# Kernel tuning notes

Measured on AMD Instinct MI355X. Metric: run time of the kernel, lower is better.

## Reference

```python
import jax, jax.numpy as jnp
import numpy as np

THRESH = 0.5   # global `thresh` used by ActFun
LENS = 0.5     # global `lens` (surrogate width)
DECAY = 0.25   # LIFNode init_decay
INV_STD = 1.0 / float(np.sqrt(1.0 + 1e-5))  # BN eval: running_mean=0, running_var=1
HEADS = 8
WINDOW = 8

@jax.custom_vjp
def act_fun(x):
    return (x > THRESH).astype(x.dtype)

def _act_fwd(x):
    return act_fun(x), x

def _act_bwd(x, g):
    temp = (jnp.abs(x - THRESH) < LENS).astype(g.dtype) / (2.0 * LENS)
    return (g * temp,)

act_fun.defvjp(_act_fwd, _act_bwd)

def lif(x):
    # x: [T, ...]; mem = x[0]; mem_t = mem_{t-1}*decay*(1-spike_{t-1}.detach()) + x_t
    spike0 = act_fun(x[0])
    def step(carry, xi):
        mem_prev, spike_prev = carry
        mem = mem_prev * DECAY * (1.0 - jax.lax.stop_gradient(spike_prev)) + xi
        spike = act_fun(mem)
        return (mem, spike), spike
    _, spikes = jax.lax.scan(step, (x[0], spike0), x[1:])
    return jnp.concatenate([spike0[None], spikes], axis=0)

def bn_eval(x, gamma, beta):
    # BatchNorm2d eval over channel D (last dim of [T,B,L,D]) with default running stats
    return x * (INV_STD * gamma) + beta

def linear(x, w, b):
    # torch nn.Linear: y = x @ w.T + b, w: [out, in]
    return jnp.einsum('tbld,ed->tble', x, w) + b


def setup_inputs() -> dict:
    key = jax.random.key(0)
    ks = jax.random.split(key, 12)
    T, B, L, D = 4, 4, 1024, 512
    s = 0.02
    inp = {
        'x': jax.random.normal(ks[0], (T, B, L, D), dtype=jnp.float32),
        'pos_bias': jax.random.uniform(ks[1], (L, L), dtype=jnp.float32),
        'q_w': jax.random.normal(ks[2], (D, D), dtype=jnp.float32) * s,
        'q_b': jnp.zeros((D,), jnp.float32),
        'q_g': jnp.ones((D,), jnp.float32),
        'q_beta': jnp.zeros((D,), jnp.float32),
        'k_w': jax.random.normal(ks[3], (D, D), dtype=jnp.float32) * s,
        'k_b': jnp.zeros((D,), jnp.float32),
        'k_g': jnp.ones((D,), jnp.float32),
        'k_beta': jnp.zeros((D,), jnp.float32),
        'v_w': jax.random.normal(ks[4], (D, D), dtype=jnp.float32) * s,
        'v_b': jnp.zeros((D,), jnp.float32),
        'v_g': jnp.ones((D,), jnp.float32),
        'v_beta': jnp.zeros((D,), jnp.float32),
        'last_w': jax.random.normal(ks[5], (D, D), dtype=jnp.float32) * s,
        'last_b': jnp.zeros((D,), jnp.float32),
        'last_g': jnp.ones((D,), jnp.float32),
        'last_beta': jnp.zeros((D,), jnp.float32),
    }
    return inp


def reference(x, pos_bias, q_w, q_b, q_g, q_beta, k_w, k_b, k_g, k_beta,
              v_w, v_b, v_g, v_beta, last_w, last_b, last_g, last_beta):
    T, B, L, D = x.shape
    H = HEADS
    Dh = D // H
    # local causal band: keep pos_bias[i,j] only where 0 <= i-j < WINDOW
    i = jnp.arange(L)[:, None]
    j = jnp.arange(L)[None, :]
    band = ((i - j) >= 0) & ((i - j) < WINDOW)
    pb = jnp.where(band, pos_bias[:L, :L], 0.0)  # [L, L]

    xs = lif(x)  # first_lif
    q = lif(bn_eval(linear(xs, q_w, q_b), q_g, q_beta))
    k = lif(bn_eval(linear(xs, k_w, k_b), k_g, k_beta))
    v = lif(bn_eval(linear(xs, v_w, v_b), v_g, v_beta))

    # [T,B,L,D] -> [T,B,L,H,Dh] -> [B,H,L,T,Dh] -> [B,H,L,T*Dh]
    qh = q.reshape(T, B, L, H, Dh).transpose(1, 3, 2, 0, 4).reshape(B, H, L, T * Dh)
    kv = (k * v).reshape(T, B, L, H, Dh).transpose(1, 3, 2, 0, 4).reshape(B, H, L, T * Dh)

    attn = jnp.einsum('ij,bhjd->bhid', pb, kv)  # local-window positional mixing
    out = qh * attn
    out = out.reshape(B, H, L, T, Dh).transpose(3, 0, 2, 1, 4).reshape(T, B, L, D)
    out = lif(out)  # attn_lif
    out = bn_eval(linear(out, last_w, last_b), last_g, last_beta)
    return out
```

## Files before the change

### kernel.cpp

```cpp
#include <hip/hip_runtime.h>
#include <stdint.h>


#define T_ 4
#define B_ 4
#define L_ 1024
#define D_ 512
#define BI_ (B_*L_)
#define STRIDE4 (B_*L_*D_/4)
#define INV_STD 0.9999950000374997f
#define EPS_FLAG 1e-3f
#define LIST_CAP 5000000u

typedef unsigned int   u32;
typedef unsigned char  u8;
typedef int i32x4 __attribute__((ext_vector_type(4)));

static __device__ __forceinline__ float spike_of(float m) {
  return m > 0.5f ? 1.0f : 0.0f;
}

__device__ __forceinline__ void gll16(const void* g, void* l) {
  __builtin_amdgcn_global_load_lds(
      (const __attribute__((address_space(1))) u32*)g,
      (__attribute__((address_space(3))) u32*)l, 16, 0, 0);
}

__global__ __launch_bounds__(256) void k_wsplit(const float* __restrict__ qw,
    const float* __restrict__ kw, const float* __restrict__ vw,
    const float* __restrict__ lw, u8* __restrict__ Wq,
    float* __restrict__ scl, u32* __restrict__ cnt) {
  if (blockIdx.x == 0 && threadIdx.x == 0) *cnt = 0;
  int gid = blockIdx.x * 4 + (threadIdx.x >> 6);
  int mat = gid >> 9, e = gid & 511;
  int lane = threadIdx.x & 63;
  const float* W = mat == 0 ? qw : mat == 1 ? kw : mat == 2 ? vw : lw;
  const float4* w4 = (const float4*)(W + (size_t)e * 512 + lane * 8);
  float4 wa = w4[0], wb = w4[1];
  float w[8] = {wa.x, wa.y, wa.z, wa.w, wb.x, wb.y, wb.z, wb.w};
  float am = 0.f;
#pragma unroll
  for (int j = 0; j < 8; ++j) am = fmaxf(am, fabsf(w[j]));
#pragma unroll
  for (int off = 1; off < 64; off <<= 1)
    am = fmaxf(am, __shfl_xor(am, off, 64));
  float s1 = am > 0.f ? am * (1.0f / 127.0f) : 1.0f;
  float s2 = s1 * (1.0f / 254.0f);
  float inv1 = 1.0f / s1, inv2 = 1.0f / s2;
  u32 p1lo = 0, p1hi = 0, p2lo = 0, p2hi = 0;
#pragma unroll
  for (int j = 0; j < 8; ++j) {
    float q1 = rintf(w[j] * inv1);
    q1 = fminf(127.f, fmaxf(-127.f, q1));
    float r = w[j] - s1 * q1;
    float q2 = rintf(r * inv2);
    q2 = fminf(127.f, fmaxf(-127.f, q2));
    u32 b1 = (u32)(u8)(signed char)(int)q1;
    u32 b2 = (u32)(u8)(signed char)(int)q2;
    if (j < 4) { p1lo |= b1 << (j * 8); p2lo |= b2 << (j * 8); }
    else       { p1hi |= b1 << ((j - 4) * 8); p2hi |= b2 << ((j - 4) * 8); }
  }
  u8* base = Wq + (size_t)mat * 524288 + (size_t)e * 512 + lane * 8;
  *(uint2*)base             = make_uint2(p1lo, p1hi);
  *(uint2*)(base + 262144)  = make_uint2(p2lo, p2hi);
  if (lane == 0) {
    scl[mat * 1024 + e] = s1;
    scl[mat * 1024 + 512 + e] = s2;
  }
}

__global__ __launch_bounds__(256) void k_lif_first(const float* __restrict__ x,
                                                   u8* __restrict__ xsb) {
  int idx = blockIdx.x * 256 + threadIdx.x;
  if (idx >= STRIDE4) return;
  const int bi = idx >> 7, d4 = idx & 127;
  const float4* x4 = (const float4*)x;
  uchar4* o4 = (uchar4*)xsb;
  float m[4], s[4];
  float4 v = x4[idx];
  m[0] = v.x; m[1] = v.y; m[2] = v.z; m[3] = v.w;
#pragma unroll
  for (int c = 0; c < 4; ++c) s[c] = spike_of(m[c]);
  o4[(bi * 4 + 0) * 128 + d4] =
      make_uchar4((u8)s[0], (u8)s[1], (u8)s[2], (u8)s[3]);
#pragma unroll
  for (int t = 1; t < T_; ++t) {
    v = x4[idx + t * STRIDE4];
    float xv[4] = {v.x, v.y, v.z, v.w};
#pragma unroll
    for (int c = 0; c < 4; ++c) {
      m[c] = m[c] * 0.25f * (1.0f - s[c]) + xv[c];
      s[c] = spike_of(m[c]);
    }
    o4[(bi * 4 + t) * 128 + d4] =
        make_uchar4((u8)s[0], (u8)s[1], (u8)s[2], (u8)s[3]);
  }
}

__device__ __forceinline__ void gemm_core_i8(const u8* __restrict__ Ab,
    const u8* __restrict__ Wq2, int row0, int col0, int tid,
    unsigned char* sm, i32x4 (&acc0)[4][4], i32x4 (&acc1)[4][4]) {
  const u8* gsrc[12];
  int loff[12];
#pragma unroll
  for (int u = 0; u < 12; ++u) {
    if (u < 4) {
      int lin = u * 4096 + tid * 16;
      int r = lin >> 7, slot = (lin >> 4) & 7, gs = slot ^ (r & 7);
      gsrc[u] = Ab + (size_t)(row0 + r) * 512 + gs * 16;
      loff[u] = lin;
    } else {
      int lin = (u - 4) * 4096 + tid * 16;
      int plane = lin >> 14, l3 = lin & 16383;
      int r = l3 >> 7, slot = (l3 >> 4) & 7, gs = slot ^ (r & 7);
      gsrc[u] = Wq2 + (size_t)plane * 262144 + (size_t)(col0 + r) * 512 + gs * 16;
      loff[u] = 16384 + lin;
    }
  }
  const int lane = tid & 63;
  const int wid = tid >> 6;
  const int wr = wid >> 1, wc = wid & 1;
  const int la = lane & 15, lg = lane >> 4;

  int offA[4][2], offB[2][4][2];
#pragma unroll
  for (int mi = 0; mi < 4; ++mi) {
    int r = wr * 64 + mi * 16 + la;
#pragma unroll
    for (int ks = 0; ks < 2; ++ks)
      offA[mi][ks] = r * 128 + (((ks * 4 + lg) ^ (r & 7)) << 4);
  }
#pragma unroll
  for (int p = 0; p < 2; ++p)
#pragma unroll
    for (int ni = 0; ni < 4; ++ni) {
      int r = wc * 64 + ni * 16 + la;
#pragma unroll
      for (int ks = 0; ks < 2; ++ks)
        offB[p][ni][ks] = 16384 + p * 16384 + r * 128 +
                          (((ks * 4 + lg) ^ (r & 7)) << 4);
    }

#pragma unroll
  for (int a = 0; a < 4; ++a)
#pragma unroll
    for (int b = 0; b < 4; ++b) {
      acc0[a][b] = (i32x4){0, 0, 0, 0};
      acc1[a][b] = (i32x4){0, 0, 0, 0};
    }

  for (int k0 = 0; k0 < 4; ++k0) {
#pragma unroll
    for (int u = 0; u < 12; ++u) gll16(gsrc[u] + (k0 << 7), sm + loff[u]);
    __syncthreads();
    uint4 af[4][2];
#pragma unroll
    for (int mi = 0; mi < 4; ++mi)
#pragma unroll
      for (int ks = 0; ks < 2; ++ks)
        af[mi][ks] = *(const uint4*)(sm + offA[mi][ks]);
#pragma unroll
    for (int ks = 0; ks < 2; ++ks)
#pragma unroll
      for (int ni = 0; ni < 4; ++ni) {
        uint4 bf = *(const uint4*)(sm + offB[0][ni][ks]);
#pragma unroll
        for (int mi = 0; mi < 4; ++mi)
          acc0[mi][ni] = __builtin_amdgcn_mfma_i32_16x16x64_i8(
              __builtin_bit_cast(i32x4, af[mi][ks]),
              __builtin_bit_cast(i32x4, bf), acc0[mi][ni], 0, 0, 0);
      }
#pragma unroll
    for (int ks = 0; ks < 2; ++ks)
#pragma unroll
      for (int ni = 0; ni < 4; ++ni) {
        uint4 bf = *(const uint4*)(sm + offB[1][ni][ks]);
#pragma unroll
        for (int mi = 0; mi < 4; ++mi)
          acc1[mi][ni] = __builtin_amdgcn_mfma_i32_16x16x64_i8(
              __builtin_bit_cast(i32x4, af[mi][ks]),
              __builtin_bit_cast(i32x4, bf), acc1[mi][ni], 0, 0, 0);
      }
    __syncthreads();
  }
}

__global__ __launch_bounds__(256) void k_gemm_qkv(const u8* __restrict__ Ab,
    const u8* __restrict__ Wq, const float* __restrict__ scl,
    const float* __restrict__ qb2, const float* __restrict__ qg,
    const float* __restrict__ qbe,
    const float* __restrict__ kb2, const float* __restrict__ kg,
    const float* __restrict__ kbe,
    const float* __restrict__ vb2, const float* __restrict__ vg,
    const float* __restrict__ vbe,
    u8* __restrict__ qs, u8* __restrict__ ks, u8* __restrict__ vs,
    u32* __restrict__ list, u32* __restrict__ cnt) {
  __shared__ __align__(16) unsigned char sm[49152];
  const int tid = threadIdx.x;
  const int tz = blockIdx.z;
  const u8* Wp = Wq + (size_t)tz * 524288;
  const float* Bb = tz == 0 ? qb2 : tz == 1 ? kb2 : vb2;
  const float* Gg = tz == 0 ? qg  : tz == 1 ? kg  : vg;
  const float* Be = tz == 0 ? qbe : tz == 1 ? kbe : vbe;
  u8* S           = tz == 0 ? qs  : tz == 1 ? ks  : vs;

  int f = blockIdx.y * 4 + blockIdx.x;
  int tI = (f & 7) * 64 + (f >> 3);
  const int row0 = (tI >> 2) * 128;
  const int col0 = (tI & 3) * 128;

  i32x4 acc0[4][4], acc1[4][4];
  gemm_core_i8(Ab, Wp, row0, col0, tid, sm, acc0, acc1);

  const int lane = tid & 63;
  const int wid = tid >> 6;
  const int wr = wid >> 1, wc = wid & 1;
  const int la = lane & 15, lg = lane >> 4;

  u8* sm8 = sm;
#pragma unroll
  for (int ni = 0; ni < 4; ++ni) {
    int cl = wc * 64 + ni * 16 + la;
    int e = col0 + cl;
    float s1 = scl[tz * 1024 + e];
    float s2 = scl[tz * 1024 + 512 + e];
    float cs = INV_STD * Gg[e];
    float cb = Bb[e], ct = Be[e];
#pragma unroll
    for (int mi = 0; mi < 4; ++mi) {
      int rl = wr * 64 + mi * 16 + lg * 4;
      int bi = (row0 + rl) >> 2;
      float m = 0.f, s = 0.f;
      int fl = 0;
#pragma unroll
      for (int p = 0; p < 4; ++p) {
        float raw = s1 * (float)acc0[mi][ni][p] + s2 * (float)acc1[mi][ni][p];
        float pre = (raw + cb) * cs + ct;
        if (p == 0) m = pre;
        else m = m * 0.25f * (1.0f - s) + pre;
        s = spike_of(m);
        if (fabsf(m - 0.5f) < EPS_FLAG) fl = 1;
        sm8[(rl + p) * 128 + cl] = (u8)s;
      }
      if (fl) {
        u32 pos = atomicAdd(cnt, 1u);
        if (pos < LIST_CAP)
          list[pos] = ((u32)tz << 21) | (u32)(bi * 512 + e);
      }
    }
  }
  __syncthreads();
#pragma unroll
  for (int ps = 0; ps < 4; ++ps) {
    int rr = ps * 32 + (tid >> 3);
    int c16 = (tid & 7) * 16;
    uint4 vv = *(const uint4*)(sm8 + rr * 128 + c16);
    *(uint4*)(S + (size_t)(row0 + rr) * 512 + col0 + c16) = vv;
  }
}

__global__ __launch_bounds__(256) void k_gemm_out(const u8* __restrict__ Ab,
    const u8* __restrict__ Wq, const float* __restrict__ scl,
    const float* __restrict__ bias, const float* __restrict__ gamma,
    const float* __restrict__ beta, float* __restrict__ Y) {
  __shared__ __align__(16) unsigned char sm[49152];
  const int tid = threadIdx.x;
  int f = blockIdx.y * 4 + blockIdx.x;
  int tI = (f & 7) * 64 + (f >> 3);
  const int row0 = (tI >> 2) * 128;
  const int col0 = (tI & 3) * 128;

  i32x4 acc0[4][4], acc1[4][4];
  gemm_core_i8(Ab, Wq + 3 * 524288, row0, col0, tid, sm, acc0, acc1);

  const int lane = tid & 63;
  const int wid = tid >> 6;
  const int wr = wid >> 1, wc = wid & 1;
  const int la = lane & 15, lg = lane >> 4;

  float* sm32 = (float*)sm;
#pragma unroll
  for (int h = 0; h < 2; ++h) {
    if (wr == h) {
#pragma unroll
      for (int ni = 0; ni < 4; ++ni) {
        int cl = wc * 64 + ni * 16 + la;
        int e = col0 + cl;
        float s1 = scl[3 * 1024 + e];
        float s2 = scl[3 * 1024 + 512 + e];
        float cs = INV_STD * gamma[e];
        float cb = bias[e], ct = beta[e];
#pragma unroll
        for (int mi = 0; mi < 4; ++mi) {
          int rb = mi * 16 + lg * 4;
#pragma unroll
          for (int p = 0; p < 4; ++p) {
            float raw = s1 * (float)acc0[mi][ni][p] +
                        s2 * (float)acc1[mi][ni][p];
            sm32[(rb + p) * 128 + cl] = (raw + cb) * cs + ct;
          }
        }
      }
    }
    __syncthreads();
    int rl = tid >> 2;
    int q0 = (tid & 3) * 32;
    int gr = row0 + h * 64 + rl;
    int bi = gr >> 2, p = gr & 3;
    float* dst = Y + ((size_t)p * BI_ + bi) * 512 + col0 + q0;
    const float* srcl = sm32 + rl * 128 + q0;
#pragma unroll
    for (int u = 0; u < 8; ++u)
      ((uint4*)dst)[u] = ((const uint4*)srcl)[u];
    __syncthreads();
  }
}

__device__ __forceinline__ void consume32_u8(const float4 (&wb)[8],
                                             const uint4 (&ab)[2], float& c) {
#pragma unroll
  for (int u = 0; u < 8; ++u) {
    float4 w = wb[u];
    uint4 t = ab[u >> 2];
    u32 word = (u & 3) == 0 ? t.x : (u & 3) == 1 ? t.y
             : (u & 3) == 2 ? t.z : t.w;
    c += (word & 0xFFu)       ? w.x : 0.0f;
    c += (word & 0xFF00u)     ? w.y : 0.0f;
    c += (word & 0xFF0000u)   ? w.z : 0.0f;
    c += (word >> 24)         ? w.w : 0.0f;
  }
}

__global__ __launch_bounds__(128) void k_fixup_c(const u8* __restrict__ xsb,
    u8* __restrict__ qs, u8* __restrict__ ks, u8* __restrict__ vs,
    const float* __restrict__ qw, const float* __restrict__ qb2,
    const float* __restrict__ qg, const float* __restrict__ qbe,
    const float* __restrict__ kw, const float* __restrict__ kb2,
    const float* __restrict__ kg, const float* __restrict__ kbe,
    const float* __restrict__ vw, const float* __restrict__ vb2,
    const float* __restrict__ vg, const float* __restrict__ vbe,
    const u32* __restrict__ list, const u32* __restrict__ cnt) {
  u32 n = *cnt;
  if (n > LIST_CAP) n = LIST_CAP;
  u32 tot = n * 4;
  for (u32 ii = blockIdx.x * 128 + threadIdx.x; ii < tot;
       ii += gridDim.x * 128) {
    u32 i = ii >> 2;
    int t = (int)(ii & 3);
    u32 e = list[i];
    int tz = (int)(e >> 21);
    int col = (int)(e & 0x1FFFFFu);
    int bi = col >> 9, d = col & 511;
    const float* W  = tz == 0 ? qw  : tz == 1 ? kw  : vw;
    const float* Bb = tz == 0 ? qb2 : tz == 1 ? kb2 : vb2;
    const float* Gg = tz == 0 ? qg  : tz == 1 ? kg  : vg;
    const float* Be = tz == 0 ? qbe : tz == 1 ? kbe : vbe;
    u8* S           = tz == 0 ? qs  : tz == 1 ? ks  : vs;
    const float4* w4 = (const float4*)(W + (size_t)d * 512);
    const uint4*  R  = (const uint4*)(xsb + ((size_t)bi * 4 + t) * 512);

    float4 wA[8], wB[8];
    uint4 aA[2], aB[2];
#pragma unroll
    for (int u = 0; u < 8; ++u) wA[u] = w4[u];
#pragma unroll
    for (int u = 0; u < 2; ++u) aA[u] = R[u];
    float c = 0.f;
#pragma unroll
    for (int ch = 0; ch < 16; ++ch) {
      if ((ch & 1) == 0) {
        if (ch + 1 < 16) {
          int wb0 = (ch + 1) * 8, ab0 = (ch + 1) * 2;
#pragma unroll
          for (int u = 0; u < 8; ++u) wB[u] = w4[wb0 + u];
#pragma unroll
          for (int u = 0; u < 2; ++u) aB[u] = R[ab0 + u];
        }
        consume32_u8(wA, aA, c);
      } else {
        if (ch + 1 < 16) {
          int wb0 = (ch + 1) * 8, ab0 = (ch + 1) * 2;
#pragma unroll
          for (int u = 0; u < 8; ++u) wA[u] = w4[wb0 + u];
#pragma unroll
          for (int u = 0; u < 2; ++u) aA[u] = R[ab0 + u];
        }
        consume32_u8(wB, aB, c);
      }
    }
    int lane = threadIdx.x & 63;
    int qb = lane & ~3;
    float cq[4];
    cq[0] = __shfl(c, qb + 0, 64);
    cq[1] = __shfl(c, qb + 1, 64);
    cq[2] = __shfl(c, qb + 2, 64);
    cq[3] = __shfl(c, qb + 3, 64);
    float cs = INV_STD * Gg[d];
    float cb = Bb[d], ct = Be[d];
    float m = 0.f, s = 0.f;
    u8 myb = 0;
#pragma unroll
    for (int t2 = 0; t2 < 4; ++t2) {
      float pre = (cq[t2] + cb) * cs + ct;
      if (t2 == 0) m = pre;
      else m = m * 0.25f * (1.0f - s) + pre;
      s = spike_of(m);
      if (t2 == t) myb = (u8)s;
    }
    S[((size_t)bi * 4 + t) * 512 + d] = myb;
  }
}

__global__ __launch_bounds__(256) void k_attn(const u8* __restrict__ qs,
    const u8* __restrict__ ks, const u8* __restrict__ vs,
    const float* __restrict__ pos_bias, u8* __restrict__ sout) {
  int idx = blockIdx.x * 256 + threadIdx.x;
  if (idx >= STRIDE4) return;
  const int d4 = idx & 127;
  const int bi = idx >> 7;
  const int i = bi & (L_ - 1);
  const int wmax = i < 7 ? i : 7;

  float pbv[8];
  const float* pbrow = pos_bias + (size_t)i * L_ + i;
  for (int w = 0; w <= wmax; ++w) pbv[w] = pbrow[-w];

  const uchar4* k4 = (const uchar4*)ks;
  const uchar4* v4 = (const uchar4*)vs;
  const uchar4* q4 = (const uchar4*)qs;
  float pre[T_][4];

#pragma unroll
  for (int t = 0; t < T_; ++t) {
    float sum[4] = {0.f, 0.f, 0.f, 0.f};
    for (int w = wmax; w >= 0; --w) {
      int rj = ((bi - w) * 4 + t) * 128 + d4;
      uchar4 ku = k4[rj];
      uchar4 vu = v4[rj];
      sum[0] += (ku.x && vu.x) ? pbv[w] : 0.0f;
      sum[1] += (ku.y && vu.y) ? pbv[w] : 0.0f;
      sum[2] += (ku.z && vu.z) ? pbv[w] : 0.0f;
      sum[3] += (ku.w && vu.w) ? pbv[w] : 0.0f;
    }
    uchar4 qu = q4[(bi * 4 + t) * 128 + d4];
    pre[t][0] = qu.x ? sum[0] : 0.0f;
    pre[t][1] = qu.y ? sum[1] : 0.0f;
    pre[t][2] = qu.z ? sum[2] : 0.0f;
    pre[t][3] = qu.w ? sum[3] : 0.0f;
  }

  uchar4* s4 = (uchar4*)sout;
  float m[4], s[4];
#pragma unroll
  for (int c = 0; c < 4; ++c) { m[c] = pre[0][c]; s[c] = spike_of(m[c]); }
  s4[(bi * 4 + 0) * 128 + d4] =
      make_uchar4((u8)s[0], (u8)s[1], (u8)s[2], (u8)s[3]);
#pragma unroll
  for (int t = 1; t < T_; ++t) {
#pragma unroll
    for (int c = 0; c < 4; ++c) {
      m[c] = m[c] * 0.25f * (1.0f - s[c]) + pre[t][c];
      s[c] = spike_of(m[c]);
    }
    s4[(bi * 4 + t) * 128 + d4] =
        make_uchar4((u8)s[0], (u8)s[1], (u8)s[2], (u8)s[3]);
  }
}

extern "C" void kernel_launch(void* const* d_in, const int* in_sizes, int n_in,
                              void* d_out, int out_size, void* d_ws, size_t ws_size,
                              hipStream_t stream) {
  (void)in_sizes; (void)n_in; (void)out_size; (void)ws_size;
  const float* x        = (const float*)d_in[0];
  const float* pos_bias = (const float*)d_in[1];
  const float* q_w    = (const float*)d_in[2];
  const float* q_b    = (const float*)d_in[3];
  const float* q_g    = (const float*)d_in[4];
  const float* q_beta = (const float*)d_in[5];
  const float* k_w    = (const float*)d_in[6];
  const float* k_b    = (const float*)d_in[7];
  const float* k_g    = (const float*)d_in[8];
  const float* k_beta = (const float*)d_in[9];
  const float* v_w    = (const float*)d_in[10];
  const float* v_b    = (const float*)d_in[11];
  const float* v_g    = (const float*)d_in[12];
  const float* v_beta = (const float*)d_in[13];
  const float* last_w    = (const float*)d_in[14];
  const float* last_b    = (const float*)d_in[15];
  const float* last_g    = (const float*)d_in[16];
  const float* last_beta = (const float*)d_in[17];
  float* out = (float*)d_out;

  char* ws = (char*)d_ws;
  u8*    xsb  = (u8*)(ws + 0);
  u8*    qs   = (u8*)(ws + 8388608);
  u8*    ks   = (u8*)(ws + 16777216);
  u8*    vs   = (u8*)(ws + 25165824);
  u8*    sA   = (u8*)(ws + 33554432);
  u8*    Wq   = (u8*)(ws + 41943040);
  float* scl  = (float*)(ws + 46137344);
  u32*   list = (u32*)(ws + 50331648);
  u32*   cnt  = (u32*)(ws + 73400320);

  k_wsplit<<<512, 256, 0, stream>>>(q_w, k_w, v_w, last_w, Wq, scl, cnt);
  k_lif_first<<<2048, 256, 0, stream>>>(x, xsb);

  dim3 gq(4, 128, 3);
  k_gemm_qkv<<<gq, 256, 0, stream>>>(xsb, Wq, scl,
      q_b, q_g, q_beta, k_b, k_g, k_beta, v_b, v_g, v_beta,
      qs, ks, vs, list, cnt);

  k_fixup_c<<<2048, 128, 0, stream>>>(xsb, qs, ks, vs,
      q_w, q_b, q_g, q_beta, k_w, k_b, k_g, k_beta, v_w, v_b, v_g, v_beta,
      list, cnt);

  k_attn<<<2048, 256, 0, stream>>>(qs, ks, vs, pos_bias, sA);

  dim3 gg(4, 128);
  k_gemm_out<<<gg, 256, 0, stream>>>(sA, Wq, scl,
                                     last_b, last_g, last_beta, out);
}
```

Before: 330.4 us.

## Replace LDS-staged int8 GEMM with register-direct loads from MFMA-ready weight layout

Weights are pre-packed into a fragment-ordered layout (64-column blocks, lane-group interleaved) so each wave can load its MFMA B operands straight from global memory. The QKV and output GEMMs drop LDS staging and syncthreads and use a register double-buffered loop over K, with each wave owning 64 rows by 64 columns. Epilogues now write spikes and outputs directly with scattered byte/float stores instead of staging through LDS for coalesced writes. This trades LDS traffic and barriers for less data reuse across waves and uncoalesced output stores.

```diff
diff --git a/kernel.cpp b/kernel.cpp
--- a/kernel.cpp
+++ b/kernel.cpp
@@ -18,12 +18,6 @@
 
 static __device__ __forceinline__ float spike_of(float m) {
   return m > 0.5f ? 1.0f : 0.0f;
-}
-
-__device__ __forceinline__ void gll16(const void* g, void* l) {
-  __builtin_amdgcn_global_load_lds(
-      (const __attribute__((address_space(1))) u32*)g,
-      (__attribute__((address_space(3))) u32*)l, 16, 0, 0);
 }
 
 __global__ __launch_bounds__(256) void k_wsplit(const float* __restrict__ qw,
@@ -60,9 +54,10 @@
     if (j < 4) { p1lo |= b1 << (j * 8); p2lo |= b2 << (j * 8); }
     else       { p1hi |= b1 << ((j - 4) * 8); p2hi |= b2 << ((j - 4) * 8); }
   }
-  u8* base = Wq + (size_t)mat * 524288 + (size_t)e * 512 + lane * 8;
+  u8* base = Wq + (size_t)mat * 524288 + (size_t)(e >> 6) * 65536 +
+             (size_t)(lane >> 1) * 1024 + (size_t)(e & 63) * 16 + (lane & 1) * 8;
   *(uint2*)base             = make_uint2(p1lo, p1hi);
-  *(uint2*)(base + 262144)  = make_uint2(p2lo, p2hi);
+  *(uint2*)(base + 32768)   = make_uint2(p2lo, p2hi);
   if (lane == 0) {
     scl[mat * 1024 + e] = s1;
     scl[mat * 1024 + 512 + e] = s2;
@@ -97,91 +92,53 @@
   }
 }
 
-__device__ __forceinline__ void gemm_core_i8(const u8* __restrict__ Ab,
-    const u8* __restrict__ Wq2, int row0, int col0, int tid,
-    unsigned char* sm, i32x4 (&acc0)[4][4], i32x4 (&acc1)[4][4]) {
-  const u8* gsrc[12];
-  int loff[12];
-#pragma unroll
-  for (int u = 0; u < 12; ++u) {
-    if (u < 4) {
-      int lin = u * 4096 + tid * 16;
-      int r = lin >> 7, slot = (lin >> 4) & 7, gs = slot ^ (r & 7);
-      gsrc[u] = Ab + (size_t)(row0 + r) * 512 + gs * 16;
-      loff[u] = lin;
-    } else {
-      int lin = (u - 4) * 4096 + tid * 16;
-      int plane = lin >> 14, l3 = lin & 16383;
-      int r = l3 >> 7, slot = (l3 >> 4) & 7, gs = slot ^ (r & 7);
-      gsrc[u] = Wq2 + (size_t)plane * 262144 + (size_t)(col0 + r) * 512 + gs * 16;
-      loff[u] = 16384 + lin;
-    }
-  }
-  const int lane = tid & 63;
-  const int wid = tid >> 6;
-  const int wr = wid >> 1, wc = wid & 1;
-  const int la = lane & 15, lg = lane >> 4;
-
-  int offA[4][2], offB[2][4][2];
-#pragma unroll
-  for (int mi = 0; mi < 4; ++mi) {
-    int r = wr * 64 + mi * 16 + la;
-#pragma unroll
-    for (int ks = 0; ks < 2; ++ks)
-      offA[mi][ks] = r * 128 + (((ks * 4 + lg) ^ (r & 7)) << 4);
-  }
-#pragma unroll
-  for (int p = 0; p < 2; ++p)
-#pragma unroll
-    for (int ni = 0; ni < 4; ++ni) {
-      int r = wc * 64 + ni * 16 + la;
-#pragma unroll
-      for (int ks = 0; ks < 2; ++ks)
-        offB[p][ni][ks] = 16384 + p * 16384 + r * 128 +
-                          (((ks * 4 + lg) ^ (r & 7)) << 4);
-    }
-
-#pragma unroll
-  for (int a = 0; a < 4; ++a)
-#pragma unroll
-    for (int b = 0; b < 4; ++b) {
-      acc0[a][b] = (i32x4){0, 0, 0, 0};
-      acc1[a][b] = (i32x4){0, 0, 0, 0};
-    }
-
-  for (int k0 = 0; k0 < 4; ++k0) {
-#pragma unroll
-    for (int u = 0; u < 12; ++u) gll16(gsrc[u] + (k0 << 7), sm + loff[u]);
-    __syncthreads();
-    uint4 af[4][2];
-#pragma unroll
-    for (int mi = 0; mi < 4; ++mi)
-#pragma unroll
-      for (int ks = 0; ks < 2; ++ks)
-        af[mi][ks] = *(const uint4*)(sm + offA[mi][ks]);
-#pragma unroll
-    for (int ks = 0; ks < 2; ++ks)
-#pragma unroll
-      for (int ni = 0; ni < 4; ++ni) {
-        uint4 bf = *(const uint4*)(sm + offB[0][ni][ks]);
-#pragma unroll
-        for (int mi = 0; mi < 4; ++mi)
-          acc0[mi][ni] = __builtin_amdgcn_mfma_i32_16x16x64_i8(
-              __builtin_bit_cast(i32x4, af[mi][ks]),
-              __builtin_bit_cast(i32x4, bf), acc0[mi][ni], 0, 0, 0);
-      }
-#pragma unroll
-    for (int ks = 0; ks < 2; ++ks)
-#pragma unroll
-      for (int ni = 0; ni < 4; ++ni) {
-        uint4 bf = *(const uint4*)(sm + offB[1][ni][ks]);
-#pragma unroll
-        for (int mi = 0; mi < 4; ++mi)
-          acc1[mi][ni] = __builtin_amdgcn_mfma_i32_16x16x64_i8(
-              __builtin_bit_cast(i32x4, af[mi][ks]),
-              __builtin_bit_cast(i32x4, bf), acc1[mi][ni], 0, 0, 0);
-      }
-    __syncthreads();
+__device__ __forceinline__ void gemm_flat(const u8* __restrict__ Ab,
+    const u8* __restrict__ Wc, int rowbase, int la, int lg,
+    i32x4 (&acc)[4][4][2]) {
+  const u8* ap = Ab + (size_t)(rowbase + la) * 512 + lg * 16;
+  const u8* bp = Wc + lg * 1024 + la * 16;
+
+#pragma unroll
+  for (int s = 0; s < 4; ++s)
+#pragma unroll
+    for (int cf = 0; cf < 4; ++cf)
+#pragma unroll
+      for (int pl = 0; pl < 2; ++pl) acc[s][cf][pl] = (i32x4){0, 0, 0, 0};
+
+  uint4 Abuf[2][4], Bbuf[2][8];
+#pragma unroll
+  for (int s = 0; s < 4; ++s)
+    Abuf[0][s] = *(const uint4*)(ap + s * 8192);
+#pragma unroll
+  for (int cf = 0; cf < 4; ++cf)
+#pragma unroll
+    for (int pl = 0; pl < 2; ++pl)
+      Bbuf[0][cf * 2 + pl] = *(const uint4*)(bp + pl * 32768 + cf * 256);
+
+#pragma unroll
+  for (int ks = 0; ks < 8; ++ks) {
+    const int cur = ks & 1, nxt = cur ^ 1;
+    if (ks < 7) {
+#pragma unroll
+      for (int s = 0; s < 4; ++s)
+        Abuf[nxt][s] = *(const uint4*)(ap + s * 8192 + (ks + 1) * 64);
+#pragma unroll
+      for (int cf = 0; cf < 4; ++cf)
+#pragma unroll
+        for (int pl = 0; pl < 2; ++pl)
+          Bbuf[nxt][cf * 2 + pl] =
+              *(const uint4*)(bp + (ks + 1) * 4096 + pl * 32768 + cf * 256);
+    }
+#pragma unroll
+    for (int cf = 0; cf < 4; ++cf)
+#pragma unroll
+      for (int pl = 0; pl < 2; ++pl)
+#pragma unroll
+        for (int s = 0; s < 4; ++s)
+          acc[s][cf][pl] = __builtin_amdgcn_mfma_i32_16x16x64_i8(
+              __builtin_bit_cast(i32x4, Abuf[cur][s]),
+              __builtin_bit_cast(i32x4, Bbuf[cur][cf * 2 + pl]),
+              acc[s][cf][pl], 0, 0, 0);
   }
 }
 
@@ -193,54 +150,45 @@
     const float* __restrict__ kbe,
     const float* __restrict__ vb2, const float* __restrict__ vg,
     const float* __restrict__ vbe,
-    u8* __restrict__ qs, u8* __restrict__ ks, u8* __restrict__ vs,
+    u8* __restrict__ qs, u8* __restrict__ ks_, u8* __restrict__ vs,
     u32* __restrict__ list, u32* __restrict__ cnt) {
-  __shared__ __align__(16) unsigned char sm[49152];
   const int tid = threadIdx.x;
+  const int lane = tid & 63, wid = tid >> 6;
+  const int la = lane & 15, lg = lane >> 4;
+  const int colblk = blockIdx.x;
   const int tz = blockIdx.z;
-  const u8* Wp = Wq + (size_t)tz * 524288;
+  const int rowbase = (blockIdx.y * 4 + wid) * 64;
+  const u8* Wc = Wq + (size_t)tz * 524288 + (size_t)colblk * 65536;
   const float* Bb = tz == 0 ? qb2 : tz == 1 ? kb2 : vb2;
   const float* Gg = tz == 0 ? qg  : tz == 1 ? kg  : vg;
   const float* Be = tz == 0 ? qbe : tz == 1 ? kbe : vbe;
-  u8* S           = tz == 0 ? qs  : tz == 1 ? ks  : vs;
-
-  int f = blockIdx.y * 4 + blockIdx.x;
-  int tI = (f & 7) * 64 + (f >> 3);
-  const int row0 = (tI >> 2) * 128;
-  const int col0 = (tI & 3) * 128;
-
-  i32x4 acc0[4][4], acc1[4][4];
-  gemm_core_i8(Ab, Wp, row0, col0, tid, sm, acc0, acc1);
-
-  const int lane = tid & 63;
-  const int wid = tid >> 6;
-  const int wr = wid >> 1, wc = wid & 1;
-  const int la = lane & 15, lg = lane >> 4;
-
-  u8* sm8 = sm;
-#pragma unroll
-  for (int ni = 0; ni < 4; ++ni) {
-    int cl = wc * 64 + ni * 16 + la;
-    int e = col0 + cl;
+  u8* S           = tz == 0 ? qs  : tz == 1 ? ks_ : vs;
+
+  i32x4 acc[4][4][2];
+  gemm_flat(Ab, Wc, rowbase, la, lg, acc);
+
+#pragma unroll
+  for (int cf = 0; cf < 4; ++cf) {
+    int e = colblk * 64 + cf * 16 + la;
     float s1 = scl[tz * 1024 + e];
     float s2 = scl[tz * 1024 + 512 + e];
     float cs = INV_STD * Gg[e];
     float cb = Bb[e], ct = Be[e];
 #pragma unroll
-    for (int mi = 0; mi < 4; ++mi) {
-      int rl = wr * 64 + mi * 16 + lg * 4;
-      int bi = (row0 + rl) >> 2;
-      float m = 0.f, s = 0.f;
+    for (int s = 0; s < 4; ++s) {
+      int r0 = rowbase + s * 16 + lg * 4;
+      int bi = r0 >> 2;
+      float m = 0.f, sp = 0.f;
       int fl = 0;
 #pragma unroll
       for (int p = 0; p < 4; ++p) {
-        float raw = s1 * (float)acc0[mi][ni][p] + s2 * (float)acc1[mi][ni][p];
+        float raw = s1 * (float)acc[s][cf][0][p] + s2 * (float)acc[s][cf][1][p];
         float pre = (raw + cb) * cs + ct;
         if (p == 0) m = pre;
-        else m = m * 0.25f * (1.0f - s) + pre;
-        s = spike_of(m);
+        else m = m * 0.25f * (1.0f - sp) + pre;
+        sp = spike_of(m);
         if (fabsf(m - 0.5f) < EPS_FLAG) fl = 1;
-        sm8[(rl + p) * 128 + cl] = (u8)s;
+        S[(size_t)(r0 + p) * 512 + e] = (u8)sp;
       }
       if (fl) {
         u32 pos = atomicAdd(cnt, 1u);
@@ -249,70 +197,39 @@
       }
     }
   }
-  __syncthreads();
-#pragma unroll
-  for (int ps = 0; ps < 4; ++ps) {
-    int rr = ps * 32 + (tid >> 3);
-    int c16 = (tid & 7) * 16;
-    uint4 vv = *(const uint4*)(sm8 + rr * 128 + c16);
-    *(uint4*)(S + (size_t)(row0 + rr) * 512 + col0 + c16) = vv;
-  }
 }
 
 __global__ __launch_bounds__(256) void k_gemm_out(const u8* __restrict__ Ab,
     const u8* __restrict__ Wq, const float* __restrict__ scl,
     const float* __restrict__ bias, const float* __restrict__ gamma,
     const float* __restrict__ beta, float* __restrict__ Y) {
-  __shared__ __align__(16) unsigned char sm[49152];
   const int tid = threadIdx.x;
-  int f = blockIdx.y * 4 + blockIdx.x;
-  int tI = (f & 7) * 64 + (f >> 3);
-  const int row0 = (tI >> 2) * 128;
-  const int col0 = (tI & 3) * 128;
-
-  i32x4 acc0[4][4], acc1[4][4];
-  gemm_core_i8(Ab, Wq + 3 * 524288, row0, col0, tid, sm, acc0, acc1);
-
-  const int lane = tid & 63;
-  const int wid = tid >> 6;
-  const int wr = wid >> 1, wc = wid & 1;
+  const int lane = tid & 63, wid = tid >> 6;
   const int la = lane & 15, lg = lane >> 4;
-
-  float* sm32 = (float*)sm;
-#pragma unroll
-  for (int h = 0; h < 2; ++h) {
-    if (wr == h) {
-#pragma unroll
-      for (int ni = 0; ni < 4; ++ni) {
-        int cl = wc * 64 + ni * 16 + la;
-        int e = col0 + cl;
-        float s1 = scl[3 * 1024 + e];
-        float s2 = scl[3 * 1024 + 512 + e];
-        float cs = INV_STD * gamma[e];
-        float cb = bias[e], ct = beta[e];
-#pragma unroll
-        for (int mi = 0; mi < 4; ++mi) {
-          int rb = mi * 16 + lg * 4;
-#pragma unroll
-          for (int p = 0; p < 4; ++p) {
-            float raw = s1 * (float)acc0[mi][ni][p] +
-                        s2 * (float)acc1[mi][ni][p];
-            sm32[(rb + p) * 128 + cl] = (raw + cb) * cs + ct;
-          }
-        }
+  const int colblk = blockIdx.x;
+  const int rowbase = (blockIdx.y * 4 + wid) * 64;
+  const u8* Wc = Wq + 3u * 524288 + (size_t)colblk * 65536;
+
+  i32x4 acc[4][4][2];
+  gemm_flat(Ab, Wc, rowbase, la, lg, acc);
+
+#pragma unroll
+  for (int cf = 0; cf < 4; ++cf) {
+    int e = colblk * 64 + cf * 16 + la;
+    float s1 = scl[3 * 1024 + e];
+    float s2 = scl[3 * 1024 + 512 + e];
+    float cs = INV_STD * gamma[e];
+    float cb = bias[e], ct = beta[e];
+#pragma unroll
+    for (int s = 0; s < 4; ++s) {
+      int r0 = rowbase + s * 16 + lg * 4;
+      int bi = r0 >> 2;
+#pragma unroll
+      for (int p = 0; p < 4; ++p) {
+        float raw = s1 * (float)acc[s][cf][0][p] + s2 * (float)acc[s][cf][1][p];
+        Y[((size_t)p * BI_ + bi) * 512 + e] = (raw + cb) * cs + ct;
       }
     }
-    __syncthreads();
-    int rl = tid >> 2;
-    int q0 = (tid & 3) * 32;
-    int gr = row0 + h * 64 + rl;
-    int bi = gr >> 2, p = gr & 3;
-    float* dst = Y + ((size_t)p * BI_ + bi) * 512 + col0 + q0;
-    const float* srcl = sm32 + rl * 128 + q0;
-#pragma unroll
-    for (int u = 0; u < 8; ++u)
-      ((uint4*)dst)[u] = ((const uint4*)srcl)[u];
-    __syncthreads();
   }
 }
 
@@ -505,7 +422,7 @@
   k_wsplit<<<512, 256, 0, stream>>>(q_w, k_w, v_w, last_w, Wq, scl, cnt);
   k_lif_first<<<2048, 256, 0, stream>>>(x, xsb);
 
-  dim3 gq(4, 128, 3);
+  dim3 gq(8, 64, 3);
   k_gemm_qkv<<<gq, 256, 0, stream>>>(xsb, Wq, scl,
       q_b, q_g, q_beta, k_b, k_g, k_beta, v_b, v_g, v_beta,
       qs, ks, vs, list, cnt);
@@ -516,7 +433,7 @@
 
   k_attn<<<2048, 256, 0, stream>>>(qs, ks, vs, pos_bias, sA);
 
-  dim3 gg(4, 128);
+  dim3 gg(8, 64);
   k_gemm_out<<<gg, 256, 0, stream>>>(sA, Wq, scl,
                                      last_b, last_g, last_beta, out);
 }
```

New measurement: 346.2 us. 4.8% more time.

## Double-buffer int8 GEMM K-loop with async LDS loads and vmcnt waits

Applied to the files above, without the earlier changes.

Replaces the single-buffered GEMM core, which issued global-to-LDS loads and then blocked on a full barrier each step, with a double-buffered 8-step pipeline over 64-byte K slices. Each step waits on a vmcnt threshold, raises wave priority around the MFMA block, and prefetches the slice two steps ahead into the buffer just consumed. The goal is to overlap global memory latency with MFMA compute. In exchange the XOR swizzle is dropped, which may cause LDS bank conflicts, and correctness now depends on the hand-written waitcnt counts.

```diff
diff --git a/kernel.cpp b/kernel.cpp
--- a/kernel.cpp
+++ b/kernel.cpp
@@ -24,6 +24,11 @@
   __builtin_amdgcn_global_load_lds(
       (const __attribute__((address_space(1))) u32*)g,
       (__attribute__((address_space(3))) u32*)l, 16, 0, 0);
+}
+
+template <int N>
+__device__ __forceinline__ void vwait() {
+  asm volatile("s_waitcnt vmcnt(%0)" :: "n"(N) : "memory");
 }
 
 __global__ __launch_bounds__(256) void k_wsplit(const float* __restrict__ qw,
@@ -61,8 +66,8 @@
     else       { p1hi |= b1 << ((j - 4) * 8); p2hi |= b2 << ((j - 4) * 8); }
   }
   u8* base = Wq + (size_t)mat * 524288 + (size_t)e * 512 + lane * 8;
-  *(uint2*)base             = make_uint2(p1lo, p1hi);
-  *(uint2*)(base + 262144)  = make_uint2(p2lo, p2hi);
+  *(uint2*)base            = make_uint2(p1lo, p1hi);
+  *(uint2*)(base + 262144) = make_uint2(p2lo, p2hi);
   if (lane == 0) {
     scl[mat * 1024 + e] = s1;
     scl[mat * 1024 + 512 + e] = s2;
@@ -97,92 +102,93 @@
   }
 }
 
-__device__ __forceinline__ void gemm_core_i8(const u8* __restrict__ Ab,
-    const u8* __restrict__ Wq2, int row0, int col0, int tid,
-    unsigned char* sm, i32x4 (&acc0)[4][4], i32x4 (&acc1)[4][4]) {
-  const u8* gsrc[12];
-  int loff[12];
-#pragma unroll
-  for (int u = 0; u < 12; ++u) {
-    if (u < 4) {
-      int lin = u * 4096 + tid * 16;
-      int r = lin >> 7, slot = (lin >> 4) & 7, gs = slot ^ (r & 7);
-      gsrc[u] = Ab + (size_t)(row0 + r) * 512 + gs * 16;
-      loff[u] = lin;
+template <int T, int VM>
+__device__ __forceinline__ void k_step(const u8* const (&gsrc)[6],
+    const int (&loff)[6], u8* sm, const int (&offA)[4],
+    const int (&offB)[2][4], i32x4 (&acc)[4][4][2]) {
+  vwait<VM>();
+  __builtin_amdgcn_s_barrier();
+  const u8* bb = sm + (T & 1) * 24576;
+  uint4 af[4], bf[8];
+#pragma unroll
+  for (int mi = 0; mi < 4; ++mi) af[mi] = *(const uint4*)(bb + offA[mi]);
+#pragma unroll
+  for (int pl = 0; pl < 2; ++pl)
+#pragma unroll
+    for (int ni = 0; ni < 4; ++ni)
+      bf[pl * 4 + ni] = *(const uint4*)(bb + offB[pl][ni]);
+  __builtin_amdgcn_s_setprio(1);
+#pragma unroll
+  for (int pl = 0; pl < 2; ++pl)
+#pragma unroll
+    for (int ni = 0; ni < 4; ++ni)
+#pragma unroll
+      for (int mi = 0; mi < 4; ++mi)
+        acc[mi][ni][pl] = __builtin_amdgcn_mfma_i32_16x16x64_i8(
+            __builtin_bit_cast(i32x4, af[mi]),
+            __builtin_bit_cast(i32x4, bf[pl * 4 + ni]),
+            acc[mi][ni][pl], 0, 0, 0);
+  __builtin_amdgcn_s_setprio(0);
+  __builtin_amdgcn_s_barrier();
+  if constexpr (T + 2 < 8) {
+#pragma unroll
+    for (int u = 0; u < 6; ++u)
+      gll16(gsrc[u] + ((T + 2) << 6), sm + (T & 1) * 24576 + loff[u]);
+  }
+}
+
+__device__ __forceinline__ void gemm_pipe(const u8* __restrict__ Ab,
+    const u8* __restrict__ Wp, int row0, int col0, int tid,
+    u8* sm, i32x4 (&acc)[4][4][2]) {
+  const u8* gsrc[6];
+  int loff[6];
+#pragma unroll
+  for (int u = 0; u < 6; ++u) {
+    int lin = u * 4096 + tid * 16;
+    if (u < 2) {
+      int r = lin >> 6, sl = (lin >> 4) & 3;
+      gsrc[u] = Ab + (size_t)(row0 + r) * 512 + sl * 16;
     } else {
-      int lin = (u - 4) * 4096 + tid * 16;
-      int plane = lin >> 14, l3 = lin & 16383;
-      int r = l3 >> 7, slot = (l3 >> 4) & 7, gs = slot ^ (r & 7);
-      gsrc[u] = Wq2 + (size_t)plane * 262144 + (size_t)(col0 + r) * 512 + gs * 16;
-      loff[u] = 16384 + lin;
-    }
+      int b = lin - 8192;
+      int pl = b >> 13, l3 = b & 8191;
+      int r = l3 >> 6, sl = (l3 >> 4) & 3;
+      gsrc[u] = Wp + (size_t)pl * 262144 + (size_t)(col0 + r) * 512 + sl * 16;
+    }
+    loff[u] = lin;
   }
   const int lane = tid & 63;
-  const int wid = tid >> 6;
-  const int wr = wid >> 1, wc = wid & 1;
+  const int wr = (tid >> 6) >> 1, wc = (tid >> 6) & 1;
   const int la = lane & 15, lg = lane >> 4;
-
-  int offA[4][2], offB[2][4][2];
-#pragma unroll
-  for (int mi = 0; mi < 4; ++mi) {
-    int r = wr * 64 + mi * 16 + la;
-#pragma unroll
-    for (int ks = 0; ks < 2; ++ks)
-      offA[mi][ks] = r * 128 + (((ks * 4 + lg) ^ (r & 7)) << 4);
-  }
-#pragma unroll
-  for (int p = 0; p < 2; ++p)
-#pragma unroll
-    for (int ni = 0; ni < 4; ++ni) {
-      int r = wc * 64 + ni * 16 + la;
-#pragma unroll
-      for (int ks = 0; ks < 2; ++ks)
-        offB[p][ni][ks] = 16384 + p * 16384 + r * 128 +
-                          (((ks * 4 + lg) ^ (r & 7)) << 4);
-    }
+  int offA[4], offB[2][4];
+#pragma unroll
+  for (int mi = 0; mi < 4; ++mi)
+    offA[mi] = (wr * 64 + mi * 16 + la) * 64 + lg * 16;
+#pragma unroll
+  for (int pl = 0; pl < 2; ++pl)
+#pragma unroll
+    for (int ni = 0; ni < 4; ++ni)
+      offB[pl][ni] = 8192 + pl * 8192 + (wc * 64 + ni * 16 + la) * 64 + lg * 16;
 
 #pragma unroll
   for (int a = 0; a < 4; ++a)
 #pragma unroll
-    for (int b = 0; b < 4; ++b) {
-      acc0[a][b] = (i32x4){0, 0, 0, 0};
-      acc1[a][b] = (i32x4){0, 0, 0, 0};
-    }
-
-  for (int k0 = 0; k0 < 4; ++k0) {
-#pragma unroll
-    for (int u = 0; u < 12; ++u) gll16(gsrc[u] + (k0 << 7), sm + loff[u]);
-    __syncthreads();
-    uint4 af[4][2];
-#pragma unroll
-    for (int mi = 0; mi < 4; ++mi)
-#pragma unroll
-      for (int ks = 0; ks < 2; ++ks)
-        af[mi][ks] = *(const uint4*)(sm + offA[mi][ks]);
-#pragma unroll
-    for (int ks = 0; ks < 2; ++ks)
-#pragma unroll
-      for (int ni = 0; ni < 4; ++ni) {
-        uint4 bf = *(const uint4*)(sm + offB[0][ni][ks]);
-#pragma unroll
-        for (int mi = 0; mi < 4; ++mi)
-          acc0[mi][ni] = __builtin_amdgcn_mfma_i32_16x16x64_i8(
-              __builtin_bit_cast(i32x4, af[mi][ks]),
-              __builtin_bit_cast(i32x4, bf), acc0[mi][ni], 0, 0, 0);
-      }
-#pragma unroll
-    for (int ks = 0; ks < 2; ++ks)
-#pragma unroll
-      for (int ni = 0; ni < 4; ++ni) {
-        uint4 bf = *(const uint4*)(sm + offB[1][ni][ks]);
-#pragma unroll
-        for (int mi = 0; mi < 4; ++mi)
-          acc1[mi][ni] = __builtin_amdgcn_mfma_i32_16x16x64_i8(
-              __builtin_bit_cast(i32x4, af[mi][ks]),
-              __builtin_bit_cast(i32x4, bf), acc1[mi][ni], 0, 0, 0);
-      }
-    __syncthreads();
-  }
+    for (int b = 0; b < 4; ++b)
+#pragma unroll
+      for (int pl = 0; pl < 2; ++pl) acc[a][b][pl] = (i32x4){0, 0, 0, 0};
+
+#pragma unroll
+  for (int u = 0; u < 6; ++u) gll16(gsrc[u], sm + loff[u]);
+#pragma unroll
+  for (int u = 0; u < 6; ++u) gll16(gsrc[u] + 64, sm + 24576 + loff[u]);
+
+  k_step<0, 6>(gsrc, loff, sm, offA, offB, acc);
+  k_step<1, 6>(gsrc, loff, sm, offA, offB, acc);
+  k_step<2, 6>(gsrc, loff, sm, offA, offB, acc);
+  k_step<3, 6>(gsrc, loff, sm, offA, offB, acc);
+  k_step<4, 6>(gsrc, loff, sm, offA, offB, acc);
+  k_step<5, 6>(gsrc, loff, sm, offA, offB, acc);
+  k_step<6, 6>(gsrc, loff, sm, offA, offB, acc);
+  k_step<7, 0>(gsrc, loff, sm, offA, offB, acc);
 }
 
 __global__ __launch_bounds__(256) void k_gemm_qkv(const u8* __restrict__ Ab,
@@ -193,28 +199,27 @@
     const float* __restrict__ kbe,
     const float* __restrict__ vb2, const float* __restrict__ vg,
     const float* __restrict__ vbe,
-    u8* __restrict__ qs, u8* __restrict__ ks, u8* __restrict__ vs,
+    u8* __restrict__ qs, u8* __restrict__ ks_, u8* __restrict__ vs,
     u32* __restrict__ list, u32* __restrict__ cnt) {
-  __shared__ __align__(16) unsigned char sm[49152];
+  __shared__ __align__(16) u8 sm[49152];
   const int tid = threadIdx.x;
   const int tz = blockIdx.z;
   const u8* Wp = Wq + (size_t)tz * 524288;
   const float* Bb = tz == 0 ? qb2 : tz == 1 ? kb2 : vb2;
   const float* Gg = tz == 0 ? qg  : tz == 1 ? kg  : vg;
   const float* Be = tz == 0 ? qbe : tz == 1 ? kbe : vbe;
-  u8* S           = tz == 0 ? qs  : tz == 1 ? ks  : vs;
+  u8* S           = tz == 0 ? qs  : tz == 1 ? ks_ : vs;
 
   int f = blockIdx.y * 4 + blockIdx.x;
   int tI = (f & 7) * 64 + (f >> 3);
   const int row0 = (tI >> 2) * 128;
   const int col0 = (tI & 3) * 128;
 
-  i32x4 acc0[4][4], acc1[4][4];
-  gemm_core_i8(Ab, Wp, row0, col0, tid, sm, acc0, acc1);
+  i32x4 acc[4][4][2];
+  gemm_pipe(Ab, Wp, row0, col0, tid, sm, acc);
 
   const int lane = tid & 63;
-  const int wid = tid >> 6;
-  const int wr = wid >> 1, wc = wid & 1;
+  const int wr = (tid >> 6) >> 1, wc = (tid >> 6) & 1;
   const int la = lane & 15, lg = lane >> 4;
 
   u8* sm8 = sm;
@@ -230,17 +235,18 @@
     for (int mi = 0; mi < 4; ++mi) {
       int rl = wr * 64 + mi * 16 + lg * 4;
       int bi = (row0 + rl) >> 2;
-      float m = 0.f, s = 0.f;
+      float m = 0.f, sp = 0.f;
       int fl = 0;
 #pragma unroll
       for (int p = 0; p < 4; ++p) {
-        float raw = s1 * (float)acc0[mi][ni][p] + s2 * (float)acc1[mi][ni][p];
+        float raw = s1 * (float)acc[mi][ni][0][p] +
+                    s2 * (float)acc[mi][ni][1][p];
         float pre = (raw + cb) * cs + ct;
         if (p == 0) m = pre;
-        else m = m * 0.25f * (1.0f - s) + pre;
-        s = spike_of(m);
+        else m = m * 0.25f * (1.0f - sp) + pre;
+        sp = spike_of(m);
         if (fabsf(m - 0.5f) < EPS_FLAG) fl = 1;
-        sm8[(rl + p) * 128 + cl] = (u8)s;
+        sm8[(rl + p) * 128 + cl] = (u8)sp;
       }
       if (fl) {
         u32 pos = atomicAdd(cnt, 1u);
@@ -263,19 +269,18 @@
     const u8* __restrict__ Wq, const float* __restrict__ scl,
     const float* __restrict__ bias, const float* __restrict__ gamma,
     const float* __restrict__ beta, float* __restrict__ Y) {
-  __shared__ __align__(16) unsigned char sm[49152];
+  __shared__ __align__(16) u8 sm[49152];
   const int tid = threadIdx.x;
   int f = blockIdx.y * 4 + blockIdx.x;
   int tI = (f & 7) * 64 + (f >> 3);
   const int row0 = (tI >> 2) * 128;
   const int col0 = (tI & 3) * 128;
 
-  i32x4 acc0[4][4], acc1[4][4];
-  gemm_core_i8(Ab, Wq + 3 * 524288, row0, col0, tid, sm, acc0, acc1);
+  i32x4 acc[4][4][2];
+  gemm_pipe(Ab, Wq + 3u * 524288, row0, col0, tid, sm, acc);
 
   const int lane = tid & 63;
-  const int wid = tid >> 6;
-  const int wr = wid >> 1, wc = wid & 1;
+  const int wr = (tid >> 6) >> 1, wc = (tid >> 6) & 1;
   const int la = lane & 15, lg = lane >> 4;
 
   float* sm32 = (float*)sm;
@@ -295,8 +300,8 @@
           int rb = mi * 16 + lg * 4;
 #pragma unroll
           for (int p = 0; p < 4; ++p) {
-            float raw = s1 * (float)acc0[mi][ni][p] +
-                        s2 * (float)acc1[mi][ni][p];
+            float raw = s1 * (float)acc[mi][ni][0][p] +
+                        s2 * (float)acc[mi][ni][1][p];
             sm32[(rb + p) * 128 + cl] = (raw + cb) * cs + ct;
           }
         }
```

After: 331.1 us. No clear change (+0.2%).
